# Kernel optimization log

Hardware: AMD Instinct MI355X
Metric: run time of the kernel (lower is better)

The kernel has to match this reference:

```python
import jax, jax.numpy as jnp
import numpy as np

D_H, D_G, D_PROJ = 1280, 768, 256
SCALE = D_PROJ ** (-0.5)

def setup_inputs() -> dict:
    key = jax.random.key(0)
    k1, k2, k3, k4 = jax.random.split(key, 4)
    B, L, T = 8, 4096, 512
    H = jax.random.normal(k1, (B, L, D_H), dtype=jnp.float32)
    G = jax.random.normal(k2, (B, T, D_G), dtype=jnp.float32)
    attn_mask = jnp.zeros((B, L), dtype=bool)  # True = pad/ignore
    # nn.Linear weights: (out_features, in_features)
    Wk = jax.random.normal(k3, (D_PROJ, D_H), dtype=jnp.float32) * (D_H ** -0.5)
    Wq = jax.random.normal(k4, (D_PROJ, D_G), dtype=jnp.float32) * (D_G ** -0.5)
    return {"H": H, "G": G, "attn_mask": attn_mask, "Wk": Wk, "Wq": Wq}

def reference(H, G, attn_mask, Wk, Wq):
    # K = Wk(H): (B,L,P); Q = Wq(G): (B,T,P)
    K = jnp.einsum('bld,pd->blp', H, Wk)
    Q = jnp.einsum('btd,pd->btp', G, Wq)
    # scores (B,T,L); streaming two-pass softmax in the original is exactly
    # softmax over L -> compute it stably in one fused expression here.
    logits = jnp.einsum('btp,blp->btl', Q, K) * SCALE
    logits = jnp.where(attn_mask[:, None, :], -jnp.inf, logits)
    alpha = jax.nn.softmax(logits, axis=-1)
    Z = jnp.einsum('btl,bld->btd', alpha, H)  # (B,T,Dh)
    return Z
```

## Files before the change

### kernel.cpp

```cpp
#include <hip/hip_runtime.h>
#include <hip/hip_bf16.h>
#include <stdint.h>


typedef float f32x4 __attribute__((ext_vector_type(4)));
typedef short bf16x8 __attribute__((ext_vector_type(8)));

__device__ __forceinline__ unsigned short f2bf(float f) {
    __hip_bfloat16 h = __float2bfloat16(f);
    return __builtin_bit_cast(unsigned short, h);
}
__device__ __forceinline__ float bf2f(unsigned short h) {
    union { uint32_t u; float f; } v; v.u = ((uint32_t)h) << 16;
    return v.f;
}

__device__ __forceinline__ int xcdswz(int bx, int nbx) {
    int cpx = nbx >> 3;
    return (bx & 7) * cpx + (bx >> 3);
}

__device__ __forceinline__ void gload16(const unsigned short* g, unsigned short* l) {
    __builtin_amdgcn_global_load_lds(
        (const __attribute__((address_space(1))) void*)g,
        (__attribute__((address_space(3))) void*)l,
        16, 0, 0);
}

__device__ __forceinline__ int lidx(int row, int kshort) {
    return row * 40 + (((kshort >> 3) ^ ((row >> 3) & 3)) << 3) + (kshort & 7);
}

__global__ __launch_bounds__(256)
void cvt_f32_bf16(const float* __restrict__ in, unsigned short* __restrict__ out, long n4)
{
    long i = (long)blockIdx.x * 256 + threadIdx.x;
    if (i >= n4) return;
    float4 v = ((const float4*)in)[i];
    ushort4 w;
    w.x = f2bf(v.x); w.y = f2bf(v.y); w.z = f2bf(v.z); w.w = f2bf(v.w);
    ((ushort4*)out)[i] = w;
}

template<bool WRITE_HB>
__global__ __launch_bounds__(256)
void cvt_h(const float* __restrict__ H, unsigned short* __restrict__ Hbt,
           unsigned short* __restrict__ Hb)
{
    __shared__ unsigned short lT[64 * 72];
    const int ntile = 64 * 20 * 8;
    for (int tileid = blockIdx.x; tileid < ntile; tileid += gridDim.x) {
        int tmp = tileid;
        const int dt = tmp % 20; tmp /= 20;
        const int lt = tmp % 64;
        const int b  = tmp / 64;
        const int l0 = lt * 64, d0 = dt * 64;
        const float* Hs = H + ((long)b * 4096 + l0) * 1280 + d0;
        #pragma unroll
        for (int it = 0; it < 4; ++it) {
            int chunk = it * 256 + threadIdx.x;
            int lr = chunk >> 4, dc4 = (chunk & 15) << 2;
            float4 v = *(const float4*)(Hs + (long)lr * 1280 + dc4);
            unsigned short w[4] = { f2bf(v.x), f2bf(v.y), f2bf(v.z), f2bf(v.w) };
            if constexpr (WRITE_HB) {
                ushort4 wb = { w[0], w[1], w[2], w[3] };
                *(ushort4*)(Hb + ((long)b * 4096 + l0 + lr) * 1280 + d0 + dc4) = wb;
            }
            #pragma unroll
            for (int j = 0; j < 4; ++j) {
                int d = dc4 + j;
                int sl = (lr & 15) | ((((lr >> 4) ^ (d >> 2)) & 3) << 4);
                lT[d * 72 + sl] = w[j];
            }
        }
        __syncthreads();
        {
            int drow = threadIdx.x >> 2, lc = threadIdx.x & 3;
            int slc = lc ^ ((drow >> 2) & 3);
            const uint4* src = (const uint4*)(lT + drow * 72 + slc * 16);
            unsigned short* dst = Hbt + ((long)b * 1280 + d0 + drow) * 4096 + l0 + lc * 16;
            uint4 v0 = src[0], v1 = src[1];
            *(uint4*)(dst)     = v0;
            *(uint4*)(dst + 8) = v1;
        }
        __syncthreads();
    }
}

__global__ __launch_bounds__(256)
void gemm_proj(const float* __restrict__ Ap, const float* __restrict__ Bp,
               unsigned short* __restrict__ Cp, int M, int N, int K)
{
    __shared__ __align__(16) unsigned short lA[128 * 40];
    __shared__ __align__(16) unsigned short lB[128 * 40];

    const int bx = xcdswz(blockIdx.x, gridDim.x);
    const int nt = N >> 7;
    const int tm = bx / nt;
    const int tn = bx % nt;
    const int tid = threadIdx.x;
    const int lane = tid & 63, wv = tid >> 6;
    const int wr = wv >> 1, wc = wv & 1;
    const int fr = lane & 15, fk = lane >> 4;

    f32x4 acc[4][4] = {};

    for (int k0 = 0; k0 < K; k0 += 32) {
        {
            const float* A = Ap + (long)tm * 128 * K + k0;
            #pragma unroll
            for (int it = 0; it < 4; ++it) {
                int chunk = it * 256 + tid;
                int row = chunk >> 3;
                int kc  = (chunk & 7) << 2;
                const float4 v = *(const float4*)(A + (long)row * K + kc);
                ushort4 w;
                w.x = f2bf(v.x); w.y = f2bf(v.y); w.z = f2bf(v.z); w.w = f2bf(v.w);
                *(ushort4*)(&lA[lidx(row, kc)]) = w;
            }
        }
        {
            const float* B = Bp + (long)tn * 128 * K + k0;
            #pragma unroll
            for (int it = 0; it < 4; ++it) {
                int chunk = it * 256 + tid;
                int row = chunk >> 3;
                int kc  = (chunk & 7) << 2;
                const float4 v = *(const float4*)(B + (long)row * K + kc);
                ushort4 w;
                w.x = f2bf(v.x); w.y = f2bf(v.y); w.z = f2bf(v.z); w.w = f2bf(v.w);
                *(ushort4*)(&lB[lidx(row, kc)]) = w;
            }
        }
        __syncthreads();
        bf16x8 af[4], bfr[4];
        #pragma unroll
        for (int i = 0; i < 4; ++i)
            af[i] = *(const bf16x8*)(&lA[lidx(wr * 64 + i * 16 + fr, fk * 8)]);
        #pragma unroll
        for (int i = 0; i < 4; ++i)
            bfr[i] = *(const bf16x8*)(&lB[lidx(wc * 64 + i * 16 + fr, fk * 8)]);
        #pragma unroll
        for (int mi = 0; mi < 4; ++mi)
            #pragma unroll
            for (int ni = 0; ni < 4; ++ni)
                acc[mi][ni] = __builtin_amdgcn_mfma_f32_16x16x32_bf16(af[mi], bfr[ni], acc[mi][ni], 0, 0, 0);
        __syncthreads();
    }

    unsigned short* C = Cp + ((long)tm * 128) * N + (long)tn * 128;
    #pragma unroll
    for (int mi = 0; mi < 4; ++mi)
        #pragma unroll
        for (int ni = 0; ni < 4; ++ni)
            #pragma unroll
            for (int j = 0; j < 4; ++j) {
                int m = wr * 64 + mi * 16 + fk * 4 + j;
                int n = wc * 64 + ni * 16 + fr;
                C[(long)m * N + n] = f2bf(acc[mi][ni][j]);
            }
}

template<bool OF32>
__global__ __launch_bounds__(256)
void gemm_bt16d(const unsigned short* __restrict__ Ap, const unsigned short* __restrict__ Bp,
                void* __restrict__ Cp, int M, int N, int K,
                long sA, long sB, long sC, float scale)
{
    __shared__ __align__(16) unsigned short lA[2][128 * 64];
    __shared__ __align__(16) unsigned short lB[2][128 * 64];

    const int bx = xcdswz(blockIdx.x, gridDim.x);
    const int nt_ = N >> 7;
    const int tm = bx / nt_, tn = bx % nt_;
    const int b  = blockIdx.y;
    const int tid = threadIdx.x;
    const int lane = tid & 63, wv = tid >> 6;
    const int wr = wv >> 1, wc = wv & 1;
    const int fr = lane & 15, fk = lane >> 4;

    f32x4 acc[4][4] = {};

    const unsigned short* A0 = Ap + (long)b * sA + (long)tm * 128 * K;
    const unsigned short* B0 = Bp + (long)b * sB + (long)tn * 128 * K;

    #define STAGE_D(bufi, kk0)                                                   \
        _Pragma("unroll")                                                        \
        for (int q = 0; q < 4; ++q) {                                            \
            int slot = wv * 256 + q * 64 + lane;                                 \
            int row = slot >> 3, c = slot & 7;                                   \
            int kc = (c ^ (row & 7)) << 3;                                       \
            gload16(A0 + (long)row * K + (kk0) + kc,                             \
                    &lA[bufi][(size_t)(wv * 256 + q * 64) * 8]);                 \
            gload16(B0 + (long)row * K + (kk0) + kc,                             \
                    &lB[bufi][(size_t)(wv * 256 + q * 64) * 8]);                 \
        }

    const int nt = K >> 6;
    STAGE_D(0, 0)
    __syncthreads();

    for (int t = 0; t < nt; ++t) {
        const int cur = t & 1;
        if (t + 1 < nt) { STAGE_D(cur ^ 1, (t + 1) << 6) }
        const unsigned short* la = lA[cur];
        const unsigned short* lb = lB[cur];
        bf16x8 af[2][4], bfv[2][4];
        #pragma unroll
        for (int ks = 0; ks < 2; ++ks) {
            int csw = ((ks * 4 + fk) ^ (fr & 7)) << 3;
            #pragma unroll
            for (int i = 0; i < 4; ++i) {
                af[ks][i]  = *(const bf16x8*)(la + (wr * 64 + i * 16 + fr) * 64 + csw);
                bfv[ks][i] = *(const bf16x8*)(lb + (wc * 64 + i * 16 + fr) * 64 + csw);
            }
        }
        #pragma unroll
        for (int mi = 0; mi < 4; ++mi)
            #pragma unroll
            for (int ni = 0; ni < 4; ++ni)
                #pragma unroll
                for (int ks = 0; ks < 2; ++ks)
                    acc[mi][ni] = __builtin_amdgcn_mfma_f32_16x16x32_bf16(af[ks][mi], bfv[ks][ni], acc[mi][ni], 0, 0, 0);
        __syncthreads();
    }
    #undef STAGE_D

    if constexpr (OF32) {
        float* C = (float*)Cp + (long)b * sC + ((long)tm * 128) * N + (long)tn * 128;
        #pragma unroll
        for (int mi = 0; mi < 4; ++mi)
            #pragma unroll
            for (int ni = 0; ni < 4; ++ni)
                #pragma unroll
                for (int j = 0; j < 4; ++j) {
                    int m = wr * 64 + mi * 16 + fk * 4 + j;
                    int n = wc * 64 + ni * 16 + fr;
                    C[(long)m * N + n] = acc[mi][ni][j] * scale;
                }
    } else {
        unsigned short* C = (unsigned short*)Cp + (long)b * sC + ((long)tm * 128) * N + (long)tn * 128;
        #pragma unroll
        for (int mi = 0; mi < 4; ++mi)
            #pragma unroll
            for (int ni = 0; ni < 4; ++ni)
                #pragma unroll
                for (int j = 0; j < 4; ++j) {
                    int m = wr * 64 + mi * 16 + fk * 4 + j;
                    int n = wc * 64 + ni * 16 + fr;
                    C[(long)m * N + n] = f2bf(acc[mi][ni][j] * scale);
                }
    }
}

__global__ __launch_bounds__(256)
void zsplitd(const unsigned short* __restrict__ Sb, const unsigned short* __restrict__ Hbt,
             float* __restrict__ Zp)
{
    __shared__ __align__(16) unsigned short lA[2][128 * 64];
    __shared__ __align__(16) unsigned short lB[2][128 * 64];

    const int K = 4096, N = 1280, KS = 1024;
    const long nZ = (long)8 * 512 * 1280;

    const int bx = xcdswz(blockIdx.x, gridDim.x);
    const int tm = bx & 3;
    const int tn = (bx >> 2) % 10;
    const int ks = bx / 40;
    const int b  = blockIdx.y;
    const int tid = threadIdx.x;
    const int lane = tid & 63, wv = tid >> 6;
    const int wr = wv >> 1, wc = wv & 1;
    const int fr = lane & 15, fk = lane >> 4;

    f32x4 acc[4][4] = {};

    const unsigned short* A0 = Sb  + ((long)b * 512  + tm * 128) * K + ks * KS;
    const unsigned short* B0 = Hbt + ((long)b * 1280 + tn * 128) * K + ks * KS;

    #define STAGE_Z(bufi, kk0)                                                   \
        _Pragma("unroll")                                                        \
        for (int q = 0; q < 4; ++q) {                                            \
            int slot = wv * 256 + q * 64 + lane;                                 \
            int row = slot >> 3, c = slot & 7;                                   \
            int kc = (c ^ (row & 7)) << 3;                                       \
            gload16(A0 + (long)row * K + (kk0) + kc,                             \
                    &lA[bufi][(size_t)(wv * 256 + q * 64) * 8]);                 \
            gload16(B0 + (long)row * K + (kk0) + kc,                             \
                    &lB[bufi][(size_t)(wv * 256 + q * 64) * 8]);                 \
        }

    const int nt = KS >> 6;
    STAGE_Z(0, 0)
    __syncthreads();

    for (int t = 0; t < nt; ++t) {
        const int cur = t & 1;
        if (t + 1 < nt) { STAGE_Z(cur ^ 1, (t + 1) << 6) }
        const unsigned short* la = lA[cur];
        const unsigned short* lb = lB[cur];
        bf16x8 af[2][4], bfv[2][4];
        #pragma unroll
        for (int kk = 0; kk < 2; ++kk) {
            int csw = ((kk * 4 + fk) ^ (fr & 7)) << 3;
            #pragma unroll
            for (int i = 0; i < 4; ++i) {
                af[kk][i]  = *(const bf16x8*)(la + (wr * 64 + i * 16 + fr) * 64 + csw);
                bfv[kk][i] = *(const bf16x8*)(lb + (wc * 64 + i * 16 + fr) * 64 + csw);
            }
        }
        #pragma unroll
        for (int mi = 0; mi < 4; ++mi)
            #pragma unroll
            for (int ni = 0; ni < 4; ++ni)
                #pragma unroll
                for (int kk = 0; kk < 2; ++kk)
                    acc[mi][ni] = __builtin_amdgcn_mfma_f32_16x16x32_bf16(af[kk][mi], bfv[kk][ni], acc[mi][ni], 0, 0, 0);
        __syncthreads();
    }
    #undef STAGE_Z

    float* C = Zp + (long)ks * nZ + ((long)b * 512 + tm * 128) * N + tn * 128;
    #pragma unroll
    for (int mi = 0; mi < 4; ++mi)
        #pragma unroll
        for (int ni = 0; ni < 4; ++ni)
            #pragma unroll
            for (int j = 0; j < 4; ++j) {
                int m = wr * 64 + mi * 16 + fk * 4 + j;
                int n = wc * 64 + ni * 16 + fr;
                C[(long)m * N + n] = acc[mi][ni][j];
            }
}

__global__ __launch_bounds__(256)
void reduce4(const float* __restrict__ p, float* __restrict__ out, long n4)
{
    long i = (long)blockIdx.x * 256 + threadIdx.x;
    if (i >= n4) return;
    const long s = n4;
    f32x4 a = ((const f32x4*)p)[i];
    f32x4 b = ((const f32x4*)p)[i + s];
    f32x4 c = ((const f32x4*)p)[i + 2 * s];
    f32x4 d = ((const f32x4*)p)[i + 3 * s];
    ((f32x4*)out)[i] = (a + b) + (c + d);
}

__global__ __launch_bounds__(256)
void gemm_kn(const unsigned short* __restrict__ Ap, const float* __restrict__ Bp,
             float* __restrict__ Cp, int M, int N, int K,
             long sA, long sB, long sC)
{
    __shared__ __align__(16) unsigned short lA[128 * 40];
    __shared__ __align__(16) unsigned short lB[64 * 40];

    const int bx = xcdswz(blockIdx.x, gridDim.x);
    const int mt = M >> 7;
    const int tm = bx % mt;
    const int tn = bx / mt;
    const int b  = blockIdx.y;
    const int tid = threadIdx.x;
    const int lane = tid & 63, wv = tid >> 6;
    const int wr = wv >> 1, wc = wv & 1;
    const int fr = lane & 15, fk = lane >> 4;

    f32x4 acc[4][2] = {};

    const unsigned short* A0 = Ap + (long)b * sA + (long)tm * 128 * K;
    const int nn    = tid & 63;
    const int khalf = tid >> 6;

    for (int k0 = 0; k0 < K; k0 += 32) {
        #pragma unroll
        for (int it = 0; it < 2; ++it) {
            int chunk = it * 256 + tid;
            int row = chunk >> 2;
            int kc  = (chunk & 3) << 3;
            *(uint4*)(&lA[lidx(row, kc)]) = *(const uint4*)(A0 + (long)row * K + k0 + kc);
        }
        {
            const float* Bb = Bp + (long)b * sB + (long)(k0 + khalf * 8) * N + (long)tn * 64 + nn;
            unsigned short t8[8];
            #pragma unroll
            for (int kk = 0; kk < 8; ++kk)
                t8[kk] = f2bf(Bb[(long)kk * N]);
            *(uint4*)(&lB[lidx(nn, khalf * 8)]) = *(uint4*)(&t8[0]);
        }
        __syncthreads();
        bf16x8 af[4], bfr[2];
        #pragma unroll
        for (int i = 0; i < 4; ++i)
            af[i] = *(const bf16x8*)(&lA[lidx(wr * 64 + i * 16 + fr, fk * 8)]);
        #pragma unroll
        for (int i = 0; i < 2; ++i)
            bfr[i] = *(const bf16x8*)(&lB[lidx(wc * 32 + i * 16 + fr, fk * 8)]);
        #pragma unroll
        for (int mi = 0; mi < 4; ++mi)
            #pragma unroll
            for (int ni = 0; ni < 2; ++ni)
                acc[mi][ni] = __builtin_amdgcn_mfma_f32_16x16x32_bf16(af[mi], bfr[ni], acc[mi][ni], 0, 0, 0);
        __syncthreads();
    }

    float* C = Cp + (long)b * sC + ((long)tm * 128) * N + (long)tn * 64;
    #pragma unroll
    for (int mi = 0; mi < 4; ++mi)
        #pragma unroll
        for (int ni = 0; ni < 2; ++ni)
            #pragma unroll
            for (int j = 0; j < 4; ++j) {
                int m = wr * 64 + mi * 16 + fk * 4 + j;
                int n = wc * 32 + ni * 16 + fr;
                C[(long)m * N + n] = acc[mi][ni][j];
            }
}

__global__ __launch_bounds__(256)
void softmax_rows(unsigned short* __restrict__ S, const unsigned char* __restrict__ mask)
{
    const int row = blockIdx.x;
    const int b = row >> 9;
    const long base = (long)row * 4096;
    const int tid = threadIdx.x, lane = tid & 63, wv = tid >> 6;
    __shared__ float red[8];

    uint4 s0 = *(const uint4*)(S + base + tid * 16);
    uint4 s1 = *(const uint4*)(S + base + tid * 16 + 8);
    uint4 mv = *(const uint4*)(mask + (long)b * 4096 + tid * 16);
    const unsigned char* mb = (const unsigned char*)&mv;

    unsigned int words[8] = { s0.x, s0.y, s0.z, s0.w, s1.x, s1.y, s1.z, s1.w };
    float x[16];
    #pragma unroll
    for (int i = 0; i < 8; ++i) {
        x[2 * i]     = bf2f((unsigned short)(words[i] & 0xffffu));
        x[2 * i + 1] = bf2f((unsigned short)(words[i] >> 16));
    }
    #pragma unroll
    for (int i = 0; i < 16; ++i)
        if (mb[i]) x[i] = -1e30f;

    float m = x[0];
    #pragma unroll
    for (int i = 1; i < 16; ++i) m = fmaxf(m, x[i]);
    #pragma unroll
    for (int off = 32; off; off >>= 1) m = fmaxf(m, __shfl_xor(m, off));
    if (lane == 0) red[wv] = m;
    __syncthreads();
    m = fmaxf(fmaxf(red[0], red[1]), fmaxf(red[2], red[3]));

    float p[16];
    float s = 0.f;
    #pragma unroll
    for (int i = 0; i < 16; ++i) { p[i] = __expf(x[i] - m); s += p[i]; }
    #pragma unroll
    for (int off = 32; off; off >>= 1) s += __shfl_xor(s, off);
    if (lane == 0) red[4 + wv] = s;
    __syncthreads();
    s = (red[4] + red[5]) + (red[6] + red[7]);
    const float inv = 1.0f / s;

    unsigned int ow[8];
    #pragma unroll
    for (int i = 0; i < 8; ++i) {
        unsigned int lo = f2bf(p[2 * i] * inv);
        unsigned int hi = f2bf(p[2 * i + 1] * inv);
        ow[i] = lo | (hi << 16);
    }
    uint4 o0 = { ow[0], ow[1], ow[2], ow[3] };
    uint4 o1 = { ow[4], ow[5], ow[6], ow[7] };
    *(uint4*)(S + base + tid * 16)     = o0;
    *(uint4*)(S + base + tid * 16 + 8) = o1;
}

extern "C" void kernel_launch(void* const* d_in, const int* in_sizes, int n_in,
                              void* d_out, int out_size, void* d_ws, size_t ws_size,
                              hipStream_t stream)
{
    const float*         H    = (const float*)d_in[0];
    const float*         G    = (const float*)d_in[1];
    const unsigned char* mask = (const unsigned char*)d_in[2];
    const float*         Wk   = (const float*)d_in[3];
    const float*         Wq   = (const float*)d_in[4];
    float*               out  = (float*)d_out;

    const long nK = (long)8 * 4096 * 256;
    const long nQ = (long)8 * 512 * 256;
    const long nS = (long)8 * 512 * 4096;
    const long nH = (long)8 * 1280 * 4096;
    const long nW = (long)256 * 1280;
    const long nZ = (long)8 * 512 * 1280;

    unsigned short* Kb  = (unsigned short*)d_ws;
    unsigned short* Qb  = Kb + nK;
    unsigned short* Sb  = Qb + nQ;
    unsigned short* Hbt = Sb + nS;
    unsigned short* Hb  = Hbt + nH;
    unsigned short* Wkb = Hb + nH;
    float*          Zp  = (float*)Hb;

    const size_t need2 = (size_t)(nK + nQ + nS + nH + nH + nW) * 2;
    const size_t need1 = (size_t)(nK + nQ + nS + nH) * 2;

    if (ws_size >= need2) {
        cvt_f32_bf16<<<dim3(320), 256, 0, stream>>>(Wk, Wkb, nW / 4);
        cvt_h<true><<<dim3(2048), 256, 0, stream>>>(H, Hbt, Hb);
        gemm_bt16d<false><<<dim3(512, 1), 256, 0, stream>>>(
            Hb, Wkb, Kb, 32768, 256, 1280, 0, 0, 0, 1.0f);
        gemm_proj<<<dim3(64, 1), 256, 0, stream>>>(G, Wq, Qb, 4096, 256, 768);
        gemm_bt16d<false><<<dim3(128, 8), 256, 0, stream>>>(
            Qb, Kb, Sb, 512, 4096, 256,
            (long)512 * 256, (long)4096 * 256, (long)512 * 4096, 0.0625f);
        softmax_rows<<<dim3(4096), 256, 0, stream>>>(Sb, mask);
        zsplitd<<<dim3(160, 8), 256, 0, stream>>>(Sb, Hbt, Zp);
        reduce4<<<dim3(5120), 256, 0, stream>>>(Zp, out, nZ / 4);
    } else if (ws_size >= need1) {
        gemm_proj<<<dim3(512, 1), 256, 0, stream>>>(H, Wk, Kb, 32768, 256, 1280);
        gemm_proj<<<dim3(64, 1), 256, 0, stream>>>(G, Wq, Qb, 4096, 256, 768);
        cvt_h<false><<<dim3(2048), 256, 0, stream>>>(H, Hbt, nullptr);
        gemm_bt16d<false><<<dim3(128, 8), 256, 0, stream>>>(
            Qb, Kb, Sb, 512, 4096, 256,
            (long)512 * 256, (long)4096 * 256, (long)512 * 4096, 0.0625f);
        softmax_rows<<<dim3(4096), 256, 0, stream>>>(Sb, mask);
        gemm_bt16d<true><<<dim3(40, 8), 256, 0, stream>>>(
            Sb, Hbt, out, 512, 1280, 4096,
            (long)512 * 4096, (long)1280 * 4096, (long)512 * 1280, 1.0f);
    } else {
        gemm_proj<<<dim3(512, 1), 256, 0, stream>>>(H, Wk, Kb, 32768, 256, 1280);
        gemm_proj<<<dim3(64, 1), 256, 0, stream>>>(G, Wq, Qb, 4096, 256, 768);
        gemm_bt16d<false><<<dim3(128, 8), 256, 0, stream>>>(
            Qb, Kb, Sb, 512, 4096, 256,
            (long)512 * 256, (long)4096 * 256, (long)512 * 4096, 0.0625f);
        softmax_rows<<<dim3(4096), 256, 0, stream>>>(Sb, mask);
        gemm_kn<<<dim3(80, 8), 256, 0, stream>>>(
            Sb, H, out, 512, 1280, 4096,
            (long)512 * 4096, (long)4096 * 1280, (long)512 * 1280);
    }
}
```

Measured before the change: 267.9 us.

## Use 256-row 512-thread GEMM tiles for K-proj, scores, and split-K Z

```diff
diff --git a/kernel.cpp b/kernel.cpp
--- a/kernel.cpp
+++ b/kernel.cpp
@@ -44,20 +44,20 @@
 
 template<bool WRITE_HB>
 __global__ __launch_bounds__(256)
-void cvt_h(const float* __restrict__ H, unsigned short* __restrict__ Hbt,
-           unsigned short* __restrict__ Hb)
-{
-    __shared__ unsigned short lT[64 * 72];
-    const int ntile = 64 * 20 * 8;
-    for (int tileid = blockIdx.x; tileid < ntile; tileid += gridDim.x) {
-        int tmp = tileid;
+void cvt_h2(const float* __restrict__ H, unsigned short* __restrict__ Hbt,
+            unsigned short* __restrict__ Hb)
+{
+    __shared__ unsigned short lT[64][136];
+    const int ntile = 32 * 20 * 8;
+    for (int tile = blockIdx.x; tile < ntile; tile += gridDim.x) {
+        int tmp = tile;
         const int dt = tmp % 20; tmp /= 20;
-        const int lt = tmp % 64;
-        const int b  = tmp / 64;
-        const int l0 = lt * 64, d0 = dt * 64;
+        const int lt = tmp % 32;
+        const int b  = tmp / 32;
+        const int l0 = lt * 128, d0 = dt * 64;
         const float* Hs = H + ((long)b * 4096 + l0) * 1280 + d0;
         #pragma unroll
-        for (int it = 0; it < 4; ++it) {
+        for (int it = 0; it < 8; ++it) {
             int chunk = it * 256 + threadIdx.x;
             int lr = chunk >> 4, dc4 = (chunk & 15) << 2;
             float4 v = *(const float4*)(Hs + (long)lr * 1280 + dc4);
@@ -69,19 +69,20 @@
             #pragma unroll
             for (int j = 0; j < 4; ++j) {
                 int d = dc4 + j;
-                int sl = (lr & 15) | ((((lr >> 4) ^ (d >> 2)) & 3) << 4);
-                lT[d * 72 + sl] = w[j];
+                int sl = (lr & 31) | ((((lr >> 5) ^ (d & 3)) & 3) << 5);
+                lT[d][sl] = w[j];
             }
         }
         __syncthreads();
         {
             int drow = threadIdx.x >> 2, lc = threadIdx.x & 3;
-            int slc = lc ^ ((drow >> 2) & 3);
-            const uint4* src = (const uint4*)(lT + drow * 72 + slc * 16);
-            unsigned short* dst = Hbt + ((long)b * 1280 + d0 + drow) * 4096 + l0 + lc * 16;
-            uint4 v0 = src[0], v1 = src[1];
-            *(uint4*)(dst)     = v0;
-            *(uint4*)(dst + 8) = v1;
+            int seg = lc ^ (drow & 3);
+            const unsigned short* src = &lT[drow][seg * 32];
+            unsigned short* dst = Hbt + ((long)b * 1280 + d0 + drow) * 4096 + l0 + lc * 32;
+            *(uint4*)(dst +  0) = *(const uint4*)(src +  0);
+            *(uint4*)(dst +  8) = *(const uint4*)(src +  8);
+            *(uint4*)(dst + 16) = *(const uint4*)(src + 16);
+            *(uint4*)(dst + 24) = *(const uint4*)(src + 24);
         }
         __syncthreads();
     }
@@ -159,6 +160,158 @@
                 int n = wc * 64 + ni * 16 + fr;
                 C[(long)m * N + n] = f2bf(acc[mi][ni][j]);
             }
+}
+
+template<int TN, bool OF32, bool TNF>
+__global__ __launch_bounds__(512, 2)
+void gemm256(const unsigned short* __restrict__ Ap, const unsigned short* __restrict__ Bp,
+             void* __restrict__ Cp, int M, int N, int Ks, int ldA, int ldB,
+             long sA, long sB, long sC, long cSlice, float scale)
+{
+    constexpr int NB = TN / 64;
+    constexpr int AISS = 2;
+    constexpr int BISS = TN / 128;
+    __shared__ __align__(16) unsigned short lA[2][256 * 32];
+    __shared__ __align__(16) unsigned short lB[2][TN * 32];
+
+    const int mt = M >> 8;
+    const int ntn = N / TN;
+    const int bx = xcdswz(blockIdx.x, gridDim.x);
+    int tm, tn, ks;
+    if (TNF) { tn = bx % ntn; int r = bx / ntn; tm = r % mt; ks = r / mt; }
+    else     { tm = bx % mt;  int r = bx / mt;  tn = r % ntn; ks = r / ntn; }
+    const int b = blockIdx.y;
+    const int tid = threadIdx.x;
+    const int lane = tid & 63, wv = tid >> 6;
+    const int wr = wv >> 2, wc = wv & 3;
+    const int fr = lane & 15, fk = lane >> 4;
+
+    f32x4 acc[8][NB] = {};
+
+    const unsigned short* A0 = Ap + (long)b * sA + ((long)tm * 256) * ldA + (long)ks * Ks;
+    const unsigned short* B0 = Bp + (long)b * sB + ((long)tn * TN) * ldB + (long)ks * Ks;
+
+    const unsigned short* aSrc[AISS]; int aDst[AISS];
+    #pragma unroll
+    for (int q = 0; q < AISS; ++q) {
+        int slot = q * 512 + tid;
+        int row = slot >> 2, c = slot & 3;
+        aSrc[q] = A0 + (long)row * ldA + ((c ^ ((row >> 1) & 3)) << 3);
+        aDst[q] = (q * 512 + wv * 64) * 8;
+    }
+    const unsigned short* bSrc[BISS]; int bDst[BISS];
+    #pragma unroll
+    for (int q = 0; q < BISS; ++q) {
+        int slot = q * 512 + tid;
+        int row = slot >> 2, c = slot & 3;
+        bSrc[q] = B0 + (long)row * ldB + ((c ^ ((row >> 1) & 3)) << 3);
+        bDst[q] = (q * 512 + wv * 64) * 8;
+    }
+    int aOff[8], bOff[NB];
+    #pragma unroll
+    for (int mi = 0; mi < 8; ++mi) {
+        int r = wr * 128 + mi * 16 + fr;
+        aOff[mi] = r * 32 + ((fk ^ ((r >> 1) & 3)) << 3);
+    }
+    #pragma unroll
+    for (int ni = 0; ni < NB; ++ni) {
+        int r = wc * (TN / 4) + ni * 16 + fr;
+        bOff[ni] = r * 32 + ((fk ^ ((r >> 1) & 3)) << 3);
+    }
+
+    #define STG(bi, kk) do {                                                  \
+        _Pragma("unroll")                                                     \
+        for (int q = 0; q < AISS; ++q) gload16(aSrc[q] + (kk), &lA[bi][aDst[q]]); \
+        _Pragma("unroll")                                                     \
+        for (int q = 0; q < BISS; ++q) gload16(bSrc[q] + (kk), &lB[bi][bDst[q]]); \
+    } while (0)
+
+    #define WAITC() do {                                                      \
+        if constexpr (TN == 256) asm volatile("s_waitcnt vmcnt(4)" ::: "memory"); \
+        else                     asm volatile("s_waitcnt vmcnt(3)" ::: "memory"); \
+    } while (0)
+    #define WAIT0() asm volatile("s_waitcnt vmcnt(0)" ::: "memory")
+    #define BARR()  do { asm volatile("" ::: "memory");                       \
+                         __builtin_amdgcn_s_barrier();                        \
+                         asm volatile("" ::: "memory"); } while (0)
+
+    #define CMP(bi) do {                                                      \
+        bf16x8 bfv[NB];                                                       \
+        _Pragma("unroll")                                                     \
+        for (int ni = 0; ni < NB; ++ni)                                       \
+            bfv[ni] = *(const bf16x8*)(&lB[bi][bOff[ni]]);                    \
+        _Pragma("unroll")                                                     \
+        for (int mi = 0; mi < 8; ++mi) {                                      \
+            bf16x8 af = *(const bf16x8*)(&lA[bi][aOff[mi]]);                  \
+            _Pragma("unroll")                                                 \
+            for (int ni = 0; ni < NB; ++ni)                                   \
+                acc[mi][ni] = __builtin_amdgcn_mfma_f32_16x16x32_bf16(        \
+                    af, bfv[ni], acc[mi][ni], 0, 0, 0);                       \
+        }                                                                     \
+    } while (0)
+
+    const int nt = Ks >> 5;
+
+    STG(0, 0);
+    #pragma unroll 1
+    for (int t = 0; t < nt; t += 2) {
+        STG(1, (t + 1) * 32);
+        WAITC();
+        BARR();
+        CMP(0);
+        BARR();
+        if (t + 2 < nt) { STG(0, (t + 2) * 32); WAITC(); }
+        else            { WAIT0(); }
+        BARR();
+        CMP(1);
+        BARR();
+    }
+    #undef STG
+    #undef WAITC
+    #undef WAIT0
+    #undef BARR
+    #undef CMP
+
+    if constexpr (OF32) {
+        float* C = (float*)Cp + (long)ks * cSlice + (long)b * sC
+                 + ((long)tm * 256) * N + (long)tn * TN;
+        #pragma unroll
+        for (int mi = 0; mi < 8; ++mi)
+            #pragma unroll
+            for (int ni = 0; ni < NB; ++ni)
+                #pragma unroll
+                for (int j = 0; j < 4; ++j) {
+                    int m = wr * 128 + mi * 16 + fk * 4 + j;
+                    int n = wc * (TN / 4) + ni * 16 + fr;
+                    C[(long)m * N + n] = acc[mi][ni][j] * scale;
+                }
+    } else {
+        unsigned short* C = (unsigned short*)Cp + (long)ks * cSlice + (long)b * sC
+                          + ((long)tm * 256) * N + (long)tn * TN;
+        #pragma unroll
+        for (int mi = 0; mi < 8; ++mi)
+            #pragma unroll
+            for (int ni = 0; ni < NB; ++ni)
+                #pragma unroll
+                for (int j = 0; j < 4; ++j) {
+                    int m = wr * 128 + mi * 16 + fk * 4 + j;
+                    int n = wc * (TN / 4) + ni * 16 + fr;
+                    C[(long)m * N + n] = f2bf(acc[mi][ni][j] * scale);
+                }
+    }
+}
+
+__global__ __launch_bounds__(256)
+void reduce4(const float* __restrict__ p, float* __restrict__ out, long n4)
+{
+    long i = (long)blockIdx.x * 256 + threadIdx.x;
+    if (i >= n4) return;
+    const long s = n4;
+    f32x4 a = ((const f32x4*)p)[i];
+    f32x4 b = ((const f32x4*)p)[i + s];
+    f32x4 c = ((const f32x4*)p)[i + 2 * s];
+    f32x4 d = ((const f32x4*)p)[i + 3 * s];
+    ((f32x4*)out)[i] = (a + b) + (c + d);
 }
 
 template<bool OF32>
@@ -254,99 +407,6 @@
 }
 
 __global__ __launch_bounds__(256)
-void zsplitd(const unsigned short* __restrict__ Sb, const unsigned short* __restrict__ Hbt,
-             float* __restrict__ Zp)
-{
-    __shared__ __align__(16) unsigned short lA[2][128 * 64];
-    __shared__ __align__(16) unsigned short lB[2][128 * 64];
-
-    const int K = 4096, N = 1280, KS = 1024;
-    const long nZ = (long)8 * 512 * 1280;
-
-    const int bx = xcdswz(blockIdx.x, gridDim.x);
-    const int tm = bx & 3;
-    const int tn = (bx >> 2) % 10;
-    const int ks = bx / 40;
-    const int b  = blockIdx.y;
-    const int tid = threadIdx.x;
-    const int lane = tid & 63, wv = tid >> 6;
-    const int wr = wv >> 1, wc = wv & 1;
-    const int fr = lane & 15, fk = lane >> 4;
-
-    f32x4 acc[4][4] = {};
-
-    const unsigned short* A0 = Sb  + ((long)b * 512  + tm * 128) * K + ks * KS;
-    const unsigned short* B0 = Hbt + ((long)b * 1280 + tn * 128) * K + ks * KS;
-
-    #define STAGE_Z(bufi, kk0)                                                   \
-        _Pragma("unroll")                                                        \
-        for (int q = 0; q < 4; ++q) {                                            \
-            int slot = wv * 256 + q * 64 + lane;                                 \
-            int row = slot >> 3, c = slot & 7;                                   \
-            int kc = (c ^ (row & 7)) << 3;                                       \
-            gload16(A0 + (long)row * K + (kk0) + kc,                             \
-                    &lA[bufi][(size_t)(wv * 256 + q * 64) * 8]);                 \
-            gload16(B0 + (long)row * K + (kk0) + kc,                             \
-                    &lB[bufi][(size_t)(wv * 256 + q * 64) * 8]);                 \
-        }
-
-    const int nt = KS >> 6;
-    STAGE_Z(0, 0)
-    __syncthreads();
-
-    for (int t = 0; t < nt; ++t) {
-        const int cur = t & 1;
-        if (t + 1 < nt) { STAGE_Z(cur ^ 1, (t + 1) << 6) }
-        const unsigned short* la = lA[cur];
-        const unsigned short* lb = lB[cur];
-        bf16x8 af[2][4], bfv[2][4];
-        #pragma unroll
-        for (int kk = 0; kk < 2; ++kk) {
-            int csw = ((kk * 4 + fk) ^ (fr & 7)) << 3;
-            #pragma unroll
-            for (int i = 0; i < 4; ++i) {
-                af[kk][i]  = *(const bf16x8*)(la + (wr * 64 + i * 16 + fr) * 64 + csw);
-                bfv[kk][i] = *(const bf16x8*)(lb + (wc * 64 + i * 16 + fr) * 64 + csw);
-            }
-        }
-        #pragma unroll
-        for (int mi = 0; mi < 4; ++mi)
-            #pragma unroll
-            for (int ni = 0; ni < 4; ++ni)
-                #pragma unroll
-                for (int kk = 0; kk < 2; ++kk)
-                    acc[mi][ni] = __builtin_amdgcn_mfma_f32_16x16x32_bf16(af[kk][mi], bfv[kk][ni], acc[mi][ni], 0, 0, 0);
-        __syncthreads();
-    }
-    #undef STAGE_Z
-
-    float* C = Zp + (long)ks * nZ + ((long)b * 512 + tm * 128) * N + tn * 128;
-    #pragma unroll
-    for (int mi = 0; mi < 4; ++mi)
-        #pragma unroll
-        for (int ni = 0; ni < 4; ++ni)
-            #pragma unroll
-            for (int j = 0; j < 4; ++j) {
-                int m = wr * 64 + mi * 16 + fk * 4 + j;
-                int n = wc * 64 + ni * 16 + fr;
-                C[(long)m * N + n] = acc[mi][ni][j];
-            }
-}
-
-__global__ __launch_bounds__(256)
-void reduce4(const float* __restrict__ p, float* __restrict__ out, long n4)
-{
-    long i = (long)blockIdx.x * 256 + threadIdx.x;
-    if (i >= n4) return;
-    const long s = n4;
-    f32x4 a = ((const f32x4*)p)[i];
-    f32x4 b = ((const f32x4*)p)[i + s];
-    f32x4 c = ((const f32x4*)p)[i + 2 * s];
-    f32x4 d = ((const f32x4*)p)[i + 3 * s];
-    ((f32x4*)out)[i] = (a + b) + (c + d);
-}
-
-__global__ __launch_bounds__(256)
 void gemm_kn(const unsigned short* __restrict__ Ap, const float* __restrict__ Bp,
              float* __restrict__ Cp, int M, int N, int K,
              long sA, long sB, long sC)
@@ -504,20 +564,22 @@
 
     if (ws_size >= need2) {
         cvt_f32_bf16<<<dim3(320), 256, 0, stream>>>(Wk, Wkb, nW / 4);
-        cvt_h<true><<<dim3(2048), 256, 0, stream>>>(H, Hbt, Hb);
-        gemm_bt16d<false><<<dim3(512, 1), 256, 0, stream>>>(
-            Hb, Wkb, Kb, 32768, 256, 1280, 0, 0, 0, 1.0f);
+        cvt_h2<true><<<dim3(2560), 256, 0, stream>>>(H, Hbt, Hb);
+        gemm256<128, false, true><<<dim3(256, 1), 512, 0, stream>>>(
+            Hb, Wkb, Kb, 32768, 256, 1280, 1280, 1280, 0, 0, 0, 0, 1.0f);
         gemm_proj<<<dim3(64, 1), 256, 0, stream>>>(G, Wq, Qb, 4096, 256, 768);
-        gemm_bt16d<false><<<dim3(128, 8), 256, 0, stream>>>(
-            Qb, Kb, Sb, 512, 4096, 256,
-            (long)512 * 256, (long)4096 * 256, (long)512 * 4096, 0.0625f);
+        gemm256<256, false, false><<<dim3(32, 8), 512, 0, stream>>>(
+            Qb, Kb, Sb, 512, 4096, 256, 256, 256,
+            (long)512 * 256, (long)4096 * 256, (long)512 * 4096, 0, 0.0625f);
         softmax_rows<<<dim3(4096), 256, 0, stream>>>(Sb, mask);
-        zsplitd<<<dim3(160, 8), 256, 0, stream>>>(Sb, Hbt, Zp);
+        gemm256<256, true, false><<<dim3(40, 8), 512, 0, stream>>>(
+            Sb, Hbt, Zp, 512, 1280, 1024, 4096, 4096,
+            (long)512 * 4096, (long)1280 * 4096, (long)512 * 1280, nZ, 1.0f);
         reduce4<<<dim3(5120), 256, 0, stream>>>(Zp, out, nZ / 4);
     } else if (ws_size >= need1) {
         gemm_proj<<<dim3(512, 1), 256, 0, stream>>>(H, Wk, Kb, 32768, 256, 1280);
         gemm_proj<<<dim3(64, 1), 256, 0, stream>>>(G, Wq, Qb, 4096, 256, 768);
-        cvt_h<false><<<dim3(2048), 256, 0, stream>>>(H, Hbt, nullptr);
+        cvt_h2<false><<<dim3(2560), 256, 0, stream>>>(H, Hbt, nullptr);
         gemm_bt16d<false><<<dim3(128, 8), 256, 0, stream>>>(
             Qb, Kb, Sb, 512, 4096, 256,
             (long)512 * 256, (long)4096 * 256, (long)512 * 4096, 0.0625f);
```

Result: no change. 270.3 us (+0.9%).
